# Performance work log

Hardware: AMD Instinct MI355X
Metric: run time of the kernel (lower is better)

Reference implementation:

```python
import jax, jax.numpy as jnp
import numpy as np

N = 100000  # nodes
E = 1000000  # edges
IN_DIM, HID_DIM, OUT_DIM = 64, 128, 2
BN_EPS = 1e-5


def sage_conv(x, src, dst, W_l, W_r, b, n_nodes):
    # PyG SAGEConv: out = lin_l(mean_{j in N(i)} x_j) + lin_r(x_i)
    msg = x[src]  # [E, d] gather
    agg = jax.ops.segment_sum(msg, dst, num_segments=n_nodes)  # [N, d]
    cnt = jax.ops.segment_sum(jnp.ones((src.shape[0],), x.dtype), dst, num_segments=n_nodes)
    agg = agg / jnp.maximum(cnt, 1.0)[:, None]  # mean aggregation
    return agg @ W_l + x @ W_r + b


def batch_norm(h, gamma, beta):
    # training-mode BatchNorm1d over the node dimension (biased variance)
    mu = h.mean(axis=0)
    var = h.var(axis=0)
    return (h - mu) * jax.lax.rsqrt(var + BN_EPS) * gamma + beta


def setup_inputs() -> dict:
    key = jax.random.key(0)
    ks = jax.random.split(key, 10)
    s = lambda fan_in: 1.0 / np.sqrt(fan_in)
    return {
        "x": jax.random.normal(ks[0], (N, IN_DIM), dtype=jnp.float32),
        "edge_index": jax.random.randint(ks[1], (2, E), 0, N, dtype=jnp.int64),
        "W1l": jax.random.uniform(ks[2], (IN_DIM, HID_DIM), jnp.float32, -s(IN_DIM), s(IN_DIM)),
        "W1r": jax.random.uniform(ks[3], (IN_DIM, HID_DIM), jnp.float32, -s(IN_DIM), s(IN_DIM)),
        "b1": jax.random.uniform(ks[4], (HID_DIM,), jnp.float32, -s(IN_DIM), s(IN_DIM)),
        "gamma": jnp.ones((HID_DIM,), jnp.float32),
        "beta": jnp.zeros((HID_DIM,), jnp.float32),
        "W2l": jax.random.uniform(ks[5], (HID_DIM, OUT_DIM), jnp.float32, -s(HID_DIM), s(HID_DIM)),
        "W2r": jax.random.uniform(ks[6], (HID_DIM, OUT_DIM), jnp.float32, -s(HID_DIM), s(HID_DIM)),
        "b2": jax.random.uniform(ks[7], (OUT_DIM,), jnp.float32, -s(HID_DIM), s(HID_DIM)),
    }


def reference(x, edge_index, W1l, W1r, b1, gamma, beta, W2l, W2r, b2):
    src, dst = edge_index[0], edge_index[1]
    h = sage_conv(x, src, dst, W1l, W1r, b1, x.shape[0])
    h = batch_norm(h, gamma, beta)
    h = jax.nn.relu(h)
    # dropout is identity in deterministic/eval reference
    return sage_conv(h, src, dst, W2l, W2r, b2, x.shape[0])
```

## Files before the change

kernel.cpp:

```cpp
#include <hip/hip_runtime.h>
#include <hip/hip_bf16.h>

#define NN 100000
#define NE 1000000
#define DIN 64
#define DH 128
#define NB 98
#define CAP 16384
#define NTILES 1563

typedef __attribute__((ext_vector_type(8))) short short8;
typedef __attribute__((ext_vector_type(4))) float floatx4;

#define OFF_BN    0
#define OFF_GCUR  256
#define OFF_OFFS  384
#define OFF_CSR   (OFF_OFFS + NN + 4)
#define OFF_PLR   (OFF_CSR + NE)
#define OFF_WF    (OFF_PLR + NN * 4)
#define OFF_AGB   (OFF_WF + 8192)
#define OFF_XB    (OFF_AGB + NN * 32)
#define OFF_H     (OFF_XB + NN * 32)

static __device__ __forceinline__ float b2f(short s) {
    union { unsigned u; float f; } c;
    c.u = ((unsigned)(unsigned short)s) << 16;
    return c.f;
}

__global__ __launch_bounds__(256) void k_prep(const float* __restrict__ x,
                                              const float* __restrict__ W1l,
                                              const float* __restrict__ W1r,
                                              ushort* __restrict__ xb,
                                              ushort* __restrict__ wfrag,
                                              int* __restrict__ gcur,
                                              float* __restrict__ bnzero) {
    int t = blockIdx.x * 256 + threadIdx.x;
    if (t < NN * DIN / 8) {
        float4 a = *(const float4*)(x + (size_t)t * 8);
        float4 b = *(const float4*)(x + (size_t)t * 8 + 4);
        __hip_bfloat16 o[8];
        o[0] = __float2bfloat16(a.x); o[1] = __float2bfloat16(a.y);
        o[2] = __float2bfloat16(a.z); o[3] = __float2bfloat16(a.w);
        o[4] = __float2bfloat16(b.x); o[5] = __float2bfloat16(b.y);
        o[6] = __float2bfloat16(b.z); o[7] = __float2bfloat16(b.w);
        *(uint4*)&xb[(size_t)t * 8] = *(uint4*)o;
    }
    if (t < 2048) {
        int ct = t >> 8, ks = (t >> 6) & 3, l = t & 63;
        int k0 = ks * 32 + (l >> 4) * 8;
        int col = ct * 16 + (l & 15);
        ushort o[8];
#pragma unroll
        for (int j = 0; j < 8; ++j) {
            int k = k0 + j;
            float v = (k < 64) ? W1l[k * DH + col] : W1r[(k - 64) * DH + col];
            __hip_bfloat16 b = __float2bfloat16(v);
            o[j] = *(ushort*)&b;
        }
        *(uint4*)&wfrag[(size_t)t * 8] = *(uint4*)o;
    }
    if (t < NB) gcur[t] = t * CAP;
    if (t < 256) bnzero[t] = 0.f;
}

__global__ __launch_bounds__(256) void k_bucket(const int* __restrict__ src,
                                                const int* __restrict__ dst,
                                                int* __restrict__ gcur,
                                                int2* __restrict__ ebuf) {
    __shared__ int lh[NB], lb[NB];
    const int tid = threadIdx.x;
    const int per = (NE + gridDim.x - 1) / gridDim.x;
    const int e0 = blockIdx.x * per, e1 = min(e0 + per, NE);
    if (tid < NB) lh[tid] = 0;
    __syncthreads();
    for (int e = e0 + tid; e < e1; e += 256)
        atomicAdd(&lh[dst[e] >> 10], 1);
    __syncthreads();
    if (tid < NB) { lb[tid] = atomicAdd(&gcur[tid], lh[tid]); lh[tid] = 0; }
    __syncthreads();
    for (int e = e0 + tid; e < e1; e += 256) {
        int d = dst[e];
        int b = d >> 10;
        int slot = lb[b] + atomicAdd(&lh[b], 1);
        ebuf[slot] = make_int2(src[e], d);
    }
}

__global__ __launch_bounds__(1024) void k_place(const int2* __restrict__ ebuf,
                                                const int* __restrict__ gcur,
                                                int* __restrict__ offs,
                                                int* __restrict__ csr) {
    __shared__ int lcnt[1024], loff[1024];
    __shared__ int sbase;
    const int b = blockIdx.x;
    const int tid = threadIdx.x;
    const int nb0 = b << 10;
    const int node_n = min(1024, NN - nb0);
    lcnt[tid] = 0;
    __syncthreads();
    if (tid == 0) {
        int acc = 0;
        for (int j = 0; j < b; ++j) acc += gcur[j] - j * CAP;
        sbase = acc;
    }
    const int e0 = b * CAP;
    const int ecnt = gcur[b] - e0;
    for (int i = tid; i < ecnt; i += 1024)
        atomicAdd(&lcnt[ebuf[e0 + i].y - nb0], 1);
    __syncthreads();
    int v = lcnt[tid];
    int sum = v;
    loff[tid] = sum;
    __syncthreads();
    for (int off = 1; off < 1024; off <<= 1) {
        int o = (tid >= off) ? loff[tid - off] : 0;
        __syncthreads();
        sum += o;
        loff[tid] = sum;
        __syncthreads();
    }
    const int excl = sum - v;
    const int base = sbase;
    if (tid < node_n) offs[nb0 + tid] = base + excl;
    if (b == NB - 1 && tid == 0) offs[NN] = NE;
    lcnt[tid] = 0;
    loff[tid] = excl;
    __syncthreads();
    for (int i = tid; i < ecnt; i += 1024) {
        int2 e = ebuf[e0 + i];
        int d = e.y - nb0;
        int slot = base + loff[d] + atomicAdd(&lcnt[d], 1);
        csr[slot] = e.x;
    }
}

__global__ __launch_bounds__(256) void k_aggv(const ushort* __restrict__ xb,
                                              const int* __restrict__ offs,
                                              const int* __restrict__ csr,
                                              ushort* __restrict__ aggb16) {
    int wid = (blockIdx.x * 256 + threadIdx.x) >> 6;
    int l = threadIdx.x & 63;
    if (wid >= NN) return;
    int beg = offs[wid];
    int deg = offs[wid + 1] - beg;
    const int g = l >> 3, d8 = l & 7;
    float a[8] = {0, 0, 0, 0, 0, 0, 0, 0};
    for (int ch = 0; ch < deg; ch += 8) {
        int j = ch + g;
        if (j < deg) {
            int sv = csr[beg + j];
            short8 v = *(const short8*)&xb[(size_t)sv * DIN + d8 * 8];
#pragma unroll
            for (int i = 0; i < 8; ++i) a[i] += b2f(v[i]);
        }
    }
#pragma unroll
    for (int i = 0; i < 8; ++i) {
        a[i] += __shfl_xor(a[i], 8);
        a[i] += __shfl_xor(a[i], 16);
        a[i] += __shfl_xor(a[i], 32);
    }
    if (g == 0) {
        float inv = 1.f / fmaxf((float)deg, 1.f);
        ushort o[8];
#pragma unroll
        for (int i = 0; i < 8; ++i) {
            __hip_bfloat16 b = __float2bfloat16(a[i] * inv);
            o[i] = *(ushort*)&b;
        }
        *(uint4*)&aggb16[(size_t)wid * DIN + d8 * 8] = *(uint4*)o;
    }
}

__global__ __launch_bounds__(256, 4) void k_mmx(const ushort* __restrict__ aggb16,
                                                const ushort* __restrict__ xb,
                                                const ushort* __restrict__ wfrag,
                                                const float* __restrict__ b1,
                                                ushort* __restrict__ hb,
                                                float* __restrict__ bnsum,
                                                float* __restrict__ bnsq) {
    __shared__ ushort sA[64 * 136];
    const int tid = threadIdx.x;
    const int l = tid & 63, w = tid >> 6;
    const int r0 = l & 15, kg = l >> 4;

    short8 bf[2][4];
#pragma unroll
    for (int c = 0; c < 2; ++c)
#pragma unroll
        for (int ks = 0; ks < 4; ++ks)
            bf[c][ks] = *(const short8*)&wfrag[(((2 * w + c) * 4 + ks) * 64 + l) * 8];

    float bias2[2];
    bias2[0] = b1[(2 * w) * 16 + r0];
    bias2[1] = b1[(2 * w + 1) * 16 + r0];

    float psum2[2] = {0.f, 0.f}, psq2[2] = {0.f, 0.f};

    for (int tile = blockIdx.x; tile < NTILES; tile += gridDim.x) {
        const int tb = tile * 64;
        __syncthreads();
#pragma unroll
        for (int i = 0; i < 4; ++i) {
            int f = tid + i * 256;
            int row = f >> 4, ch = f & 15;
            const uint4* src = (ch < 8)
                ? (const uint4*)(aggb16 + (size_t)(tb + row) * 64 + ch * 8)
                : (const uint4*)(xb + (size_t)(tb + row) * 64 + (ch - 8) * 8);
            *(uint4*)&sA[row * 136 + ch * 8] = *src;
        }
        __syncthreads();

#pragma unroll
        for (int s = 0; s < 4; ++s) {
            short8 af[4];
            const int abase = (s * 16 + r0) * 136 + kg * 8;
#pragma unroll
            for (int ks = 0; ks < 4; ++ks)
                af[ks] = *(const short8*)&sA[abase + ks * 32];
#pragma unroll
            for (int c = 0; c < 2; ++c) {
                floatx4 acc = {0.f, 0.f, 0.f, 0.f};
#pragma unroll
                for (int ks = 0; ks < 4; ++ks)
                    acc = __builtin_amdgcn_mfma_f32_16x16x32_bf16(af[ks], bf[c][ks], acc, 0, 0, 0);
                const int col = (2 * w + c) * 16 + r0;
#pragma unroll
                for (int i = 0; i < 4; ++i) {
                    int r = tb + s * 16 + kg * 4 + i;
                    if (r < NN) {
                        float o = acc[i] + bias2[c];
                        __hip_bfloat16 ob = __float2bfloat16(o);
                        hb[(size_t)r * DH + col] = *(ushort*)&ob;
                        psum2[c] += o;
                        psq2[c] += o * o;
                    }
                }
            }
        }
    }

#pragma unroll
    for (int c = 0; c < 2; ++c) {
        float s = psum2[c], q = psq2[c];
        s += __shfl_xor(s, 16); s += __shfl_xor(s, 32);
        q += __shfl_xor(q, 16); q += __shfl_xor(q, 32);
        if (kg == 0) {
            atomicAdd(&bnsum[(2 * w + c) * 16 + r0], s);
            atomicAdd(&bnsq[(2 * w + c) * 16 + r0], q);
        }
    }
}

__global__ __launch_bounds__(256) void k_proj(const ushort* __restrict__ hb,
                                              const float* __restrict__ bnsum,
                                              const float* __restrict__ bnsq,
                                              const float* __restrict__ gamma,
                                              const float* __restrict__ beta,
                                              const float* __restrict__ W2l,
                                              const float* __restrict__ W2r,
                                              float4* __restrict__ plr) {
    __shared__ float sCA[DH], sCC[DH];
    int tid = threadIdx.x;
    if (tid < DH) {
        float mu = bnsum[tid] * (1.f / NN);
        float var = bnsq[tid] * (1.f / NN) - mu * mu;
        float a = rsqrtf(var + 1e-5f) * gamma[tid];
        sCA[tid] = a;
        sCC[tid] = beta[tid] - mu * a;
    }
    __syncthreads();
    int wid = (blockIdx.x * 256 + tid) >> 6;
    int lane = tid & 63;
    if (wid >= NN) return;
    int c0 = lane * 2;
    uint hv = *(const uint*)&hb[(size_t)wid * DH + c0];
    float h0 = b2f((short)(hv & 0xffff));
    float h1 = b2f((short)(hv >> 16));
    float hb0 = fmaxf(h0 * sCA[c0] + sCC[c0], 0.f);
    float hb1 = fmaxf(h1 * sCA[c0 + 1] + sCC[c0 + 1], 0.f);
    float pl0 = hb0 * W2l[c0 * 2 + 0] + hb1 * W2l[c0 * 2 + 2];
    float pl1 = hb0 * W2l[c0 * 2 + 1] + hb1 * W2l[c0 * 2 + 3];
    float pr0 = hb0 * W2r[c0 * 2 + 0] + hb1 * W2r[c0 * 2 + 2];
    float pr1 = hb0 * W2r[c0 * 2 + 1] + hb1 * W2r[c0 * 2 + 3];
#pragma unroll
    for (int off = 32; off > 0; off >>= 1) {
        pl0 += __shfl_down(pl0, off);
        pl1 += __shfl_down(pl1, off);
        pr0 += __shfl_down(pr0, off);
        pr1 += __shfl_down(pr1, off);
    }
    if (lane == 0) plr[wid] = make_float4(pl0, pl1, pr0, pr1);
}

__global__ __launch_bounds__(256) void k_out(const float4* __restrict__ plr,
                                             const int* __restrict__ offs,
                                             const int* __restrict__ csr,
                                             const float* __restrict__ b2,
                                             float* __restrict__ out) {
    int d = blockIdx.x * 256 + threadIdx.x;
    if (d >= NN) return;
    int beg = offs[d];
    int deg = offs[d + 1] - beg;
    const float2* pl2 = (const float2*)plr;
    float s0 = 0.f, s1 = 0.f;
    int i = 0;
    for (; i + 4 <= deg; i += 4) {
        int n0 = csr[beg + i], n1 = csr[beg + i + 1];
        int n2 = csr[beg + i + 2], n3 = csr[beg + i + 3];
        float2 p0 = pl2[(size_t)n0 * 2];
        float2 p1 = pl2[(size_t)n1 * 2];
        float2 p2 = pl2[(size_t)n2 * 2];
        float2 p3 = pl2[(size_t)n3 * 2];
        s0 += (p0.x + p1.x) + (p2.x + p3.x);
        s1 += (p0.y + p1.y) + (p2.y + p3.y);
    }
    for (; i < deg; ++i) {
        float2 p = pl2[(size_t)csr[beg + i] * 2];
        s0 += p.x;
        s1 += p.y;
    }
    float inv = 1.f / fmaxf((float)deg, 1.f);
    float4 me = plr[d];
    out[(size_t)d * 2 + 0] = s0 * inv + me.z + b2[0];
    out[(size_t)d * 2 + 1] = s1 * inv + me.w + b2[1];
}

extern "C" void kernel_launch(void* const* d_in, const int* in_sizes, int n_in,
                              void* d_out, int out_size, void* d_ws, size_t ws_size,
                              hipStream_t stream) {
    const float* x = (const float*)d_in[0];
    const int* ei = (const int*)d_in[1];
    const float* W1l = (const float*)d_in[2];
    const float* W1r = (const float*)d_in[3];
    const float* b1 = (const float*)d_in[4];
    const float* gamma = (const float*)d_in[5];
    const float* beta = (const float*)d_in[6];
    const float* W2l = (const float*)d_in[7];
    const float* W2r = (const float*)d_in[8];
    const float* b2 = (const float*)d_in[9];
    float* out = (float*)d_out;
    float* ws = (float*)d_ws;
    int* wsi = (int*)d_ws;

    const int* src = ei;
    const int* dst = ei + NE;

    float* bnsum = ws + OFF_BN;
    float* bnsq = ws + OFF_BN + 128;
    int* gcur = wsi + OFF_GCUR;
    int* offs = wsi + OFF_OFFS;
    int* csr = wsi + OFF_CSR;
    float4* plr = (float4*)(ws + OFF_PLR);
    ushort* wfrag = (ushort*)(ws + OFF_WF);
    ushort* aggb16 = (ushort*)(ws + OFF_AGB);
    ushort* xb = (ushort*)(ws + OFF_XB);
    ushort* hb = (ushort*)(ws + OFF_H);
    int2* ebuf = (int2*)(ws + OFF_H);

    k_prep<<<(NN * DIN / 8 + 255) / 256, 256, 0, stream>>>(x, W1l, W1r, xb, wfrag, gcur, ws + OFF_BN);
    k_bucket<<<256, 256, 0, stream>>>(src, dst, gcur, ebuf);
    k_place<<<NB, 1024, 0, stream>>>(ebuf, gcur, offs, csr);
    k_aggv<<<(NN * 64 + 255) / 256, 256, 0, stream>>>(xb, offs, csr, aggb16);
    k_mmx<<<782, 256, 0, stream>>>(aggb16, xb, wfrag, b1, hb, bnsum, bnsq);
    k_proj<<<(NN + 3) / 4, 256, 0, stream>>>(hb, bnsum, bnsq, gamma, beta, W2l, W2r, plr);
    k_out<<<(NN + 255) / 256, 256, 0, stream>>>(plr, offs, csr, b2, out);
}
```

Before: 227.6 us.

## Fuse input prep with edge bucketing and pack edge records into one int

Merges the bf16 conversion/weight-fragment prep kernel and the edge bucketing kernel into a single launch where the first 256 blocks bucket edges and the rest convert x, so the two independent stages overlap on the device. Edge records are packed as (src<<10)|(dst&1023) in a single int instead of an int2, halving ebuf traffic in bucketing and placement. Counter and BN-accumulator initialization moves to a hipMemsetAsync, gcur now holds per-bucket counts, and k_place caches them in shared memory. The packing assumes src fits in 22 bits, which holds for 100k nodes.

```diff
diff --git a/kernel.cpp b/kernel.cpp
--- a/kernel.cpp
+++ b/kernel.cpp
@@ -8,6 +8,8 @@
 #define NB 98
 #define CAP 16384
 #define NTILES 1563
+#define EDGEB 256
+#define CVTB 3125
 
 typedef __attribute__((ext_vector_type(8))) short short8;
 typedef __attribute__((ext_vector_type(4))) float floatx4;
@@ -28,86 +30,85 @@
     return c.f;
 }
 
-__global__ __launch_bounds__(256) void k_prep(const float* __restrict__ x,
-                                              const float* __restrict__ W1l,
-                                              const float* __restrict__ W1r,
-                                              ushort* __restrict__ xb,
-                                              ushort* __restrict__ wfrag,
-                                              int* __restrict__ gcur,
-                                              float* __restrict__ bnzero) {
-    int t = blockIdx.x * 256 + threadIdx.x;
-    if (t < NN * DIN / 8) {
-        float4 a = *(const float4*)(x + (size_t)t * 8);
-        float4 b = *(const float4*)(x + (size_t)t * 8 + 4);
-        __hip_bfloat16 o[8];
-        o[0] = __float2bfloat16(a.x); o[1] = __float2bfloat16(a.y);
-        o[2] = __float2bfloat16(a.z); o[3] = __float2bfloat16(a.w);
-        o[4] = __float2bfloat16(b.x); o[5] = __float2bfloat16(b.y);
-        o[6] = __float2bfloat16(b.z); o[7] = __float2bfloat16(b.w);
-        *(uint4*)&xb[(size_t)t * 8] = *(uint4*)o;
-    }
-    if (t < 2048) {
-        int ct = t >> 8, ks = (t >> 6) & 3, l = t & 63;
-        int k0 = ks * 32 + (l >> 4) * 8;
-        int col = ct * 16 + (l & 15);
-        ushort o[8];
-#pragma unroll
-        for (int j = 0; j < 8; ++j) {
-            int k = k0 + j;
-            float v = (k < 64) ? W1l[k * DH + col] : W1r[(k - 64) * DH + col];
-            __hip_bfloat16 b = __float2bfloat16(v);
-            o[j] = *(ushort*)&b;
-        }
-        *(uint4*)&wfrag[(size_t)t * 8] = *(uint4*)o;
-    }
-    if (t < NB) gcur[t] = t * CAP;
-    if (t < 256) bnzero[t] = 0.f;
-}
-
-__global__ __launch_bounds__(256) void k_bucket(const int* __restrict__ src,
-                                                const int* __restrict__ dst,
-                                                int* __restrict__ gcur,
-                                                int2* __restrict__ ebuf) {
-    __shared__ int lh[NB], lb[NB];
+__global__ __launch_bounds__(256) void k_bucketprep(const float* __restrict__ x,
+                                                    const float* __restrict__ W1l,
+                                                    const float* __restrict__ W1r,
+                                                    const int* __restrict__ src,
+                                                    const int* __restrict__ dst,
+                                                    ushort* __restrict__ xb,
+                                                    ushort* __restrict__ wfrag,
+                                                    int* __restrict__ gcur,
+                                                    int* __restrict__ ebuf) {
+    const int bid = blockIdx.x;
     const int tid = threadIdx.x;
-    const int per = (NE + gridDim.x - 1) / gridDim.x;
-    const int e0 = blockIdx.x * per, e1 = min(e0 + per, NE);
-    if (tid < NB) lh[tid] = 0;
-    __syncthreads();
-    for (int e = e0 + tid; e < e1; e += 256)
-        atomicAdd(&lh[dst[e] >> 10], 1);
-    __syncthreads();
-    if (tid < NB) { lb[tid] = atomicAdd(&gcur[tid], lh[tid]); lh[tid] = 0; }
-    __syncthreads();
-    for (int e = e0 + tid; e < e1; e += 256) {
-        int d = dst[e];
-        int b = d >> 10;
-        int slot = lb[b] + atomicAdd(&lh[b], 1);
-        ebuf[slot] = make_int2(src[e], d);
-    }
-}
-
-__global__ __launch_bounds__(1024) void k_place(const int2* __restrict__ ebuf,
+    if (bid < EDGEB) {
+        __shared__ int lh[NB], lb[NB];
+        const int per = (NE + EDGEB - 1) / EDGEB;
+        const int e0 = bid * per, e1 = min(e0 + per, NE);
+        if (tid < NB) lh[tid] = 0;
+        __syncthreads();
+        for (int e = e0 + tid; e < e1; e += 256)
+            atomicAdd(&lh[dst[e] >> 10], 1);
+        __syncthreads();
+        if (tid < NB) { lb[tid] = atomicAdd(&gcur[tid], lh[tid]); lh[tid] = 0; }
+        __syncthreads();
+        for (int e = e0 + tid; e < e1; e += 256) {
+            int d = dst[e];
+            int b = d >> 10;
+            int slot = b * CAP + lb[b] + atomicAdd(&lh[b], 1);
+            ebuf[slot] = (src[e] << 10) | (d & 1023);
+        }
+    } else {
+        int t = (bid - EDGEB) * 256 + tid;
+        if (t < NN * DIN / 8) {
+            float4 a = *(const float4*)(x + (size_t)t * 8);
+            float4 b = *(const float4*)(x + (size_t)t * 8 + 4);
+            __hip_bfloat16 o[8];
+            o[0] = __float2bfloat16(a.x); o[1] = __float2bfloat16(a.y);
+            o[2] = __float2bfloat16(a.z); o[3] = __float2bfloat16(a.w);
+            o[4] = __float2bfloat16(b.x); o[5] = __float2bfloat16(b.y);
+            o[6] = __float2bfloat16(b.z); o[7] = __float2bfloat16(b.w);
+            *(uint4*)&xb[(size_t)t * 8] = *(uint4*)o;
+        }
+        if (t < 2048) {
+            int ct = t >> 8, ks = (t >> 6) & 3, l = t & 63;
+            int k0 = ks * 32 + (l >> 4) * 8;
+            int col = ct * 16 + (l & 15);
+            ushort o[8];
+#pragma unroll
+            for (int j = 0; j < 8; ++j) {
+                int k = k0 + j;
+                float v = (k < 64) ? W1l[k * DH + col] : W1r[(k - 64) * DH + col];
+                __hip_bfloat16 b = __float2bfloat16(v);
+                o[j] = *(ushort*)&b;
+            }
+            *(uint4*)&wfrag[(size_t)t * 8] = *(uint4*)o;
+        }
+    }
+}
+
+__global__ __launch_bounds__(1024) void k_place(const int* __restrict__ ebuf,
                                                 const int* __restrict__ gcur,
                                                 int* __restrict__ offs,
                                                 int* __restrict__ csr) {
-    __shared__ int lcnt[1024], loff[1024];
+    __shared__ int lcnt[1024], loff[1024], pre[NB];
     __shared__ int sbase;
     const int b = blockIdx.x;
     const int tid = threadIdx.x;
     const int nb0 = b << 10;
     const int node_n = min(1024, NN - nb0);
+    if (tid < NB) pre[tid] = gcur[tid];
     lcnt[tid] = 0;
     __syncthreads();
     if (tid == 0) {
         int acc = 0;
-        for (int j = 0; j < b; ++j) acc += gcur[j] - j * CAP;
+        for (int j = 0; j < b; ++j) acc += pre[j];
         sbase = acc;
     }
     const int e0 = b * CAP;
-    const int ecnt = gcur[b] - e0;
+    const int ecnt = pre[b];
     for (int i = tid; i < ecnt; i += 1024)
-        atomicAdd(&lcnt[ebuf[e0 + i].y - nb0], 1);
+        atomicAdd(&lcnt[ebuf[e0 + i] & 1023], 1);
     __syncthreads();
     int v = lcnt[tid];
     int sum = v;
@@ -128,10 +129,10 @@
     loff[tid] = excl;
     __syncthreads();
     for (int i = tid; i < ecnt; i += 1024) {
-        int2 e = ebuf[e0 + i];
-        int d = e.y - nb0;
+        int e = ebuf[e0 + i];
+        int d = e & 1023;
         int slot = base + loff[d] + atomicAdd(&lcnt[d], 1);
-        csr[slot] = e.x;
+        csr[slot] = e >> 10;
     }
 }
 
@@ -357,10 +358,11 @@
     ushort* aggb16 = (ushort*)(ws + OFF_AGB);
     ushort* xb = (ushort*)(ws + OFF_XB);
     ushort* hb = (ushort*)(ws + OFF_H);
-    int2* ebuf = (int2*)(ws + OFF_H);
-
-    k_prep<<<(NN * DIN / 8 + 255) / 256, 256, 0, stream>>>(x, W1l, W1r, xb, wfrag, gcur, ws + OFF_BN);
-    k_bucket<<<256, 256, 0, stream>>>(src, dst, gcur, ebuf);
+    int* ebuf = (int*)(ws + OFF_H);
+
+    hipMemsetAsync(ws, 0, (256 + NB) * sizeof(float), stream);
+
+    k_bucketprep<<<EDGEB + CVTB, 256, 0, stream>>>(x, W1l, W1r, src, dst, xb, wfrag, gcur, ebuf);
     k_place<<<NB, 1024, 0, stream>>>(ebuf, gcur, offs, csr);
     k_aggv<<<(NN * 64 + 255) / 256, 256, 0, stream>>>(xb, offs, csr, aggb16);
     k_mmx<<<782, 256, 0, stream>>>(aggb16, xb, wfrag, b1, hb, bnsum, bnsq);
```

Measured after the change: 224.9 us. Within noise of the previous version (-1.2%).
